# Optimization experiments

Hardware: AMD Instinct MI355X
Metric: run time of the kernel (lower is better)

The kernel has to match this reference:

```python
import jax, jax.numpy as jnp
import numpy as np

N, E, B = 50000, 500000, 2048
IN, ED, H, OUT, P = 64, 16, 64, 64, 1
L, T = 3, 3  # num_layers, num_timesteps
NS = 0.01  # leaky_relu negative slope used throughout AttentiveFP


def _seg_softmax(logits, seg, num):
    # numerically-stable softmax over segments (PyG `softmax`), eps matches PyG
    m = jax.ops.segment_max(logits, seg, num_segments=num)
    e = jnp.exp(logits - m[seg])
    s = jax.ops.segment_sum(e, seg, num_segments=num)
    return e / (s[seg] + 1e-16)


def _gru(xin, h, wx, wh, bx, bh):
    # torch.nn.GRUCell
    gx = xin @ wx.T + bx
    gh = h @ wh.T + bh
    xr, xz, xn = jnp.split(gx, 3, axis=-1)
    hr, hz, hn = jnp.split(gh, 3, axis=-1)
    r = jax.nn.sigmoid(xr + hr)
    z = jax.nn.sigmoid(xz + hz)
    n = jnp.tanh(xn + r * hn)
    return (1.0 - z) * n + z * h


def _forward(x, edge_attr, lin1_w, lin1_b, gate_lin1_w, gate_lin2_w, gate_att_l, gate_att_r, gate_bias,
             gru0_wx, gru0_wh, gru0_bx, gru0_bh,
             atom_lin_w, atom_att_src, atom_att_dst, atom_bias,
             atom_gru_wx, atom_gru_wh, atom_gru_bx, atom_gru_bh,
             mol_lin_w, mol_att_src, mol_att_dst, mol_bias,
             mol_gru_wx, mol_gru_wh, mol_gru_bx, mol_gru_bh,
             lin2_w, lin2_b, ln_g, ln_b, h1_w, h1_b, h2_w, h2_b, h3_w, h3_b,
             edge_index, batch):
    src, dst = edge_index[0], edge_index[1]  # messages flow src -> dst
    x = jax.nn.leaky_relu(x @ lin1_w.T + lin1_b, NS)  # [N, H]
    # --- GATEConv (edge-featured attention) ---
    xj = x[src]  # [E, H]
    e = jax.nn.leaky_relu(jnp.concatenate([xj, edge_attr], axis=-1) @ gate_lin1_w.T, NS)
    alpha = jax.nn.leaky_relu(e @ gate_att_l + x[dst] @ gate_att_r, NS)  # [E]
    alpha = _seg_softmax(alpha, dst, N)
    h = jax.ops.segment_sum((xj @ gate_lin2_w.T) * alpha[:, None], dst, num_segments=N) + gate_bias
    x = jax.nn.relu(_gru(jax.nn.elu(h), x, gru0_wx, gru0_wh, gru0_bx, gru0_bh))
    # --- (num_layers-1) GATConv + GRU layers ---
    for l in range(L - 1):
        xl = x @ atom_lin_w[l].T  # [N, H]
        a = jax.nn.leaky_relu((xl @ atom_att_src[l])[src] + (xl @ atom_att_dst[l])[dst], NS)
        a = _seg_softmax(a, dst, N)
        h = jax.ops.segment_sum(xl[src] * a[:, None], dst, num_segments=N) + atom_bias[l]
        x = jax.nn.relu(_gru(jax.nn.elu(h), x,
                             atom_gru_wx[l], atom_gru_wh[l], atom_gru_bx[l], atom_gru_bh[l]))
    # --- attentive readout over num_timesteps ---
    out = jax.nn.relu(jax.ops.segment_sum(x, batch, num_segments=B))  # [B, H]
    xs = x @ mol_lin_w.T          # bipartite GATConv source transform (fixed)
    a_src = xs @ mol_att_src      # [N]
    for _ in range(T):
        a = jax.nn.leaky_relu(a_src + ((out @ mol_lin_w.T) @ mol_att_dst)[batch], NS)
        a = _seg_softmax(a, batch, B)
        h = jax.nn.elu(jax.ops.segment_sum(xs * a[:, None], batch, num_segments=B) + mol_bias)
        out = jax.nn.relu(_gru(h, out, mol_gru_wx, mol_gru_wh, mol_gru_bx, mol_gru_bh))
    emb = out @ lin2_w.T + lin2_b  # [B, OUT]
    mu = jnp.mean(emb, -1, keepdims=True)
    var = jnp.var(emb, -1, keepdims=True)
    y = (emb - mu) / jnp.sqrt(var + 1e-5) * ln_g + ln_b
    y = jax.nn.relu(y @ h1_w.T + h1_b)
    y = jax.nn.relu(y @ h2_w.T + h2_b)
    return y @ h3_w.T + h3_b  # [B, P]


def setup_inputs() -> dict:
    key = jax.random.key(0)
    ks = iter(jax.random.split(key, 64))
    def w(*s):
        return jax.random.normal(next(ks), s, jnp.float32) * 0.05
    return dict(
        x=jax.random.normal(next(ks), (N, IN), jnp.float32),
        edge_attr=jax.random.normal(next(ks), (E, ED), jnp.float32),
        lin1_w=w(H, IN), lin1_b=w(H),
        gate_lin1_w=w(H, IN + ED), gate_lin2_w=w(H, H),
        gate_att_l=w(H), gate_att_r=w(H), gate_bias=w(H),
        gru0_wx=w(3 * H, H), gru0_wh=w(3 * H, H), gru0_bx=w(3 * H), gru0_bh=w(3 * H),
        atom_lin_w=w(L - 1, H, H), atom_att_src=w(L - 1, H), atom_att_dst=w(L - 1, H), atom_bias=w(L - 1, H),
        atom_gru_wx=w(L - 1, 3 * H, H), atom_gru_wh=w(L - 1, 3 * H, H),
        atom_gru_bx=w(L - 1, 3 * H), atom_gru_bh=w(L - 1, 3 * H),
        mol_lin_w=w(H, H), mol_att_src=w(H), mol_att_dst=w(H), mol_bias=w(H),
        mol_gru_wx=w(3 * H, H), mol_gru_wh=w(3 * H, H), mol_gru_bx=w(3 * H), mol_gru_bh=w(3 * H),
        lin2_w=w(OUT, H), lin2_b=w(OUT),
        ln_g=jnp.ones((OUT,), jnp.float32), ln_b=jnp.zeros((OUT,), jnp.float32),
        h1_w=w(64, OUT), h1_b=w(64), h2_w=w(64, 64), h2_b=w(64), h3_w=w(P, 64), h3_b=w(P),
        edge_index=jax.random.randint(next(ks), (2, E), 0, N, dtype=jnp.int32),
        batch=jnp.sort(jax.random.randint(next(ks), (N,), 0, B, dtype=jnp.int32)),
    )


def reference(x, edge_attr, lin1_w, lin1_b, gate_lin1_w, gate_lin2_w, gate_att_l, gate_att_r, gate_bias, gru0_wx, gru0_wh, gru0_bx, gru0_bh, atom_lin_w, atom_att_src, atom_att_dst, atom_bias, atom_gru_wx, atom_gru_wh, atom_gru_bx, atom_gru_bh, mol_lin_w, mol_att_src, mol_att_dst, mol_bias, mol_gru_wx, mol_gru_wh, mol_gru_bx, mol_gru_bh, lin2_w, lin2_b, ln_g, ln_b, h1_w, h1_b, h2_w, h2_b, h3_w, h3_b, edge_index, batch):
    return _forward(x, edge_attr, lin1_w, lin1_b, gate_lin1_w, gate_lin2_w, gate_att_l, gate_att_r, gate_bias, gru0_wx, gru0_wh, gru0_bx, gru0_bh, atom_lin_w, atom_att_src, atom_att_dst, atom_bias, atom_gru_wx, atom_gru_wh, atom_gru_bx, atom_gru_bh, mol_lin_w, mol_att_src, mol_att_dst, mol_bias, mol_gru_wx, mol_gru_wh, mol_gru_bx, mol_gru_bh, lin2_w, lin2_b, ln_g, ln_b, h1_w, h1_b, h2_w, h2_b, h3_w, h3_b, edge_index, batch)
```

## Files before the change

### kernel.cpp

```cpp
#include <hip/hip_runtime.h>
#include <cfloat>

#define THREADS 256

#define PIN(x) asm volatile("" : "+v"(x))

__device__ __forceinline__ float lrelu01(float v){ return v > 0.f ? v : 0.01f * v; }
__device__ __forceinline__ float reluf(float v){ return v > 0.f ? v : 0.f; }
__device__ __forceinline__ float sigmf(float v){ return 1.f / (1.f + __expf(-v)); }
__device__ __forceinline__ float tanhfast(float v){
    float t = __expf(-2.f * fabsf(v));
    float r = (1.f - t) / (1.f + t);
    return v < 0.f ? -r : r;
}
__device__ __forceinline__ float eluf(float v){ return v > 0.f ? v : __expf(v) - 1.f; }
__device__ __forceinline__ float wmaxf(float v){
    #pragma unroll
    for (int o = 32; o > 0; o >>= 1) v = fmaxf(v, __shfl_xor(v, o, 64));
    return v;
}
__device__ __forceinline__ float wsumf(float v){
    #pragma unroll
    for (int o = 32; o > 0; o >>= 1) v += __shfl_xor(v, o, 64);
    return v;
}

template<int ACT>
__device__ __forceinline__ float actf(float v){
    if (ACT == 1) return lrelu01(v);
    if (ACT == 2) return reluf(v);
    return v;
}

__device__ __forceinline__ void stage_tile(const float* __restrict__ src, float* lds,
                                           int tid, int validf4){
    #pragma unroll
    for (int j = 0; j < 4; ++j){
        int idx = tid + j * 256;
        if (idx < validf4){
            __builtin_amdgcn_global_load_lds(
                (const __attribute__((address_space(1))) void*)(src + (size_t)idx * 4),
                (__attribute__((address_space(3))) void*)(lds + (size_t)idx * 4),
                16, 0, 0);
        }
    }
}

__global__ void k_hist(const int* __restrict__ dst, int* __restrict__ cnt, int E){
    int e = blockIdx.x * blockDim.x + threadIdx.x;
    if (e < E) atomicAdd(&cnt[dst[e]], 1);
}

__global__ void k_scan1(const int* __restrict__ cnt, int* __restrict__ rowptr,
                        int* __restrict__ bsum, int N){
    const int tid = threadIdx.x;
    int i = blockIdx.x * 1024 + tid;
    int v = (i < N) ? cnt[i] : 0;
    int lane = tid & 63, wv = tid >> 6;
    int s = v;
    #pragma unroll
    for (int o = 1; o < 64; o <<= 1){
        int u = __shfl_up(s, o, 64);
        if (lane >= o) s += u;
    }
    __shared__ int wsum[16];
    if (lane == 63) wsum[wv] = s;
    __syncthreads();
    if (wv == 0 && lane < 16){
        int ws = wsum[lane];
        #pragma unroll
        for (int o = 1; o < 16; o <<= 1){
            int u = __shfl_up(ws, o, 64);
            if (lane >= o) ws += u;
        }
        wsum[lane] = ws;
    }
    __syncthreads();
    int woff = wv ? wsum[wv - 1] : 0;
    int incl = s + woff;
    if (i < N) rowptr[i] = incl - v;
    if (tid == 1023) bsum[blockIdx.x] = incl;
}

__global__ void k_scan2(int* __restrict__ bsum, int* __restrict__ rowptr, int NB, int N){
    const int tid = threadIdx.x;
    int v = (tid < NB) ? bsum[tid] : 0;
    int lane = tid & 63, wv = tid >> 6;
    int s = v;
    #pragma unroll
    for (int o = 1; o < 64; o <<= 1){
        int u = __shfl_up(s, o, 64);
        if (lane >= o) s += u;
    }
    __shared__ int wsum[16];
    if (lane == 63) wsum[wv] = s;
    __syncthreads();
    if (wv == 0 && lane < 16){
        int ws = wsum[lane];
        #pragma unroll
        for (int o = 1; o < 16; o <<= 1){
            int u = __shfl_up(ws, o, 64);
            if (lane >= o) ws += u;
        }
        wsum[lane] = ws;
    }
    __syncthreads();
    int woff = wv ? wsum[wv - 1] : 0;
    int incl = s + woff;
    if (tid < NB) bsum[tid] = incl - v;
    if (tid == 1023) rowptr[N] = incl;
}

__global__ void k_scan3(int* __restrict__ rowptr, const int* __restrict__ bsum, int N){
    int i = blockIdx.x * 1024 + threadIdx.x;
    if (i < N) rowptr[i] += bsum[blockIdx.x];
}

__global__ void k_scatter(const int* __restrict__ dst, const int* __restrict__ srcv,
                          const int* __restrict__ rowptr, int* __restrict__ cnt2,
                          int* __restrict__ srcC, int* __restrict__ slot, int E){
    int e = blockIdx.x * blockDim.x + threadIdx.x;
    if (e < E){
        int d = dst[e];
        int p = rowptr[d] + atomicAdd(&cnt2[d], 1);
        srcC[p] = srcv[e];
        slot[e] = p;
    }
}

__global__ void k_browptr(const int* __restrict__ batch, int* __restrict__ rp, int N, int B){
    int n = blockIdx.x * blockDim.x + threadIdx.x;
    if (n >= N) return;
    int b = batch[n];
    int bp = (n == 0) ? -1 : batch[n - 1];
    for (int g = bp + 1; g <= b; ++g) rp[g] = n;
    if (n == N - 1){ for (int g = b + 1; g <= B; ++g) rp[g] = N; }
}

template<int ACT, int NDOT>
__global__ __launch_bounds__(THREADS, 3)
void k_mm64t(const float* __restrict__ in, const float* __restrict__ W, int ldw,
             const float* __restrict__ bias, float* __restrict__ out,
             const float* __restrict__ v0, const float* __restrict__ v1,
             float* __restrict__ o0, float* __restrict__ o1, int rows){
    __shared__ float tile[2][4096];
    const int tid  = threadIdx.x;
    const int lane = tid & 63;
    const int wv   = tid >> 6;
    float w[64];
    #pragma unroll
    for (int k = 0; k < 64; k += 4){
        float4 t4 = *(const float4*)(W + (size_t)lane * ldw + k);
        w[k] = t4.x; w[k+1] = t4.y; w[k+2] = t4.z; w[k+3] = t4.w;
    }
    #pragma unroll
    for (int k = 0; k < 64; ++k) PIN(w[k]);
    const float bb  = bias ? bias[lane] : 0.f;
    const float vl0 = (NDOT > 0) ? v0[lane] : 0.f;
    const float vl1 = (NDOT > 1) ? v1[lane] : 0.f;
    const int ntiles = (rows + 63) >> 6;
    const int totf4  = rows * 16;
    int t = blockIdx.x;
    if (t >= ntiles) return;
    stage_tile(in + (size_t)t * 4096, tile[0], tid, min(1024, totf4 - t * 1024));
    __syncthreads();
    int b = 0;
    while (t < ntiles){
        int tn = t + gridDim.x;
        if (tn < ntiles)
            stage_tile(in + (size_t)tn * 4096, tile[b ^ 1], tid, min(1024, totf4 - tn * 1024));
        #pragma unroll 4
        for (int r = 0; r < 16; ++r){
            int row = wv * 16 + r;
            int g = t * 64 + row;
            const float4* rp = (const float4*)&tile[b][row * 64];
            float a0 = bb, a1 = 0.f, a2 = 0.f, a3 = 0.f;
            #pragma unroll
            for (int kk = 0; kk < 16; ++kk){
                float4 q = rp[kk];
                a0 = fmaf(q.x, w[kk*4],   a0);
                a1 = fmaf(q.y, w[kk*4+1], a1);
                a2 = fmaf(q.z, w[kk*4+2], a2);
                a3 = fmaf(q.w, w[kk*4+3], a3);
            }
            float v = actf<ACT>((a0 + a1) + (a2 + a3));
            if (g < rows){
                out[(size_t)g * 64 + lane] = v;
                if (NDOT > 0){
                    float s0 = wsumf(v * vl0);
                    float s1 = (NDOT > 1) ? wsumf(v * vl1) : 0.f;
                    if (lane == 0){ o0[g] = s0; if (NDOT > 1) o1[g] = s1; }
                }
            }
        }
        __syncthreads();
        b ^= 1; t = tn;
    }
}

__global__ __launch_bounds__(THREADS, 3)
void k_gru_x_t(const float* __restrict__ xin, const float* __restrict__ wx,
               const float* __restrict__ bx,
               float* __restrict__ Rt, float* __restrict__ Zt, float* __restrict__ XN,
               int rows){
    __shared__ float tile[2][4096];
    const int c = blockIdx.y;
    const int tid  = threadIdx.x;
    const int lane = tid & 63;
    const int wv   = tid >> 6;
    float w[64];
    const float* wp = wx + (size_t)(c * 64 + lane) * 64;
    #pragma unroll
    for (int k = 0; k < 64; k += 4){
        float4 t4 = *(const float4*)(wp + k);
        w[k] = t4.x; w[k+1] = t4.y; w[k+2] = t4.z; w[k+3] = t4.w;
    }
    #pragma unroll
    for (int k = 0; k < 64; ++k) PIN(w[k]);
    const float bb = bx[c * 64 + lane];
    float* T = (c == 0) ? Rt : ((c == 1) ? Zt : XN);
    const int ntiles = (rows + 63) >> 6;
    const int totf4  = rows * 16;
    int t = blockIdx.x;
    if (t >= ntiles) return;
    stage_tile(xin + (size_t)t * 4096, tile[0], tid, min(1024, totf4 - t * 1024));
    __syncthreads();
    int b = 0;
    while (t < ntiles){
        int tn = t + gridDim.x;
        if (tn < ntiles)
            stage_tile(xin + (size_t)tn * 4096, tile[b ^ 1], tid, min(1024, totf4 - tn * 1024));
        #pragma unroll 4
        for (int r = 0; r < 16; ++r){
            int row = wv * 16 + r;
            int g = t * 64 + row;
            const float4* rp = (const float4*)&tile[b][row * 64];
            float a0 = bb, a1 = 0.f, a2 = 0.f, a3 = 0.f;
            #pragma unroll
            for (int kk = 0; kk < 16; ++kk){
                float4 q = rp[kk];
                a0 = fmaf(q.x, w[kk*4],   a0);
                a1 = fmaf(q.y, w[kk*4+1], a1);
                a2 = fmaf(q.z, w[kk*4+2], a2);
                a3 = fmaf(q.w, w[kk*4+3], a3);
            }
            if (g < rows) T[(size_t)g * 64 + lane] = (a0 + a1) + (a2 + a3);
        }
        __syncthreads();
        b ^= 1; t = tn;
    }
}

__global__ __launch_bounds__(THREADS, 3)
void k_gru_hsig_t(const float* __restrict__ xp, const float* __restrict__ wh,
                  const float* __restrict__ bh,
                  float* __restrict__ Rt, float* __restrict__ Zt, int rows){
    __shared__ float tile[2][4096];
    const int c = blockIdx.y;
    const int tid  = threadIdx.x;
    const int lane = tid & 63;
    const int wv   = tid >> 6;
    float w[64];
    const float* wp = wh + (size_t)(c * 64 + lane) * 64;
    #pragma unroll
    for (int k = 0; k < 64; k += 4){
        float4 t4 = *(const float4*)(wp + k);
        w[k] = t4.x; w[k+1] = t4.y; w[k+2] = t4.z; w[k+3] = t4.w;
    }
    #pragma unroll
    for (int k = 0; k < 64; ++k) PIN(w[k]);
    const float bb = bh[c * 64 + lane];
    float* T = c ? Zt : Rt;
    const int ntiles = (rows + 63) >> 6;
    const int totf4  = rows * 16;
    int t = blockIdx.x;
    if (t >= ntiles) return;
    stage_tile(xp + (size_t)t * 4096, tile[0], tid, min(1024, totf4 - t * 1024));
    __syncthreads();
    int b = 0;
    while (t < ntiles){
        int tn = t + gridDim.x;
        if (tn < ntiles)
            stage_tile(xp + (size_t)tn * 4096, tile[b ^ 1], tid, min(1024, totf4 - tn * 1024));
        #pragma unroll 4
        for (int r = 0; r < 16; ++r){
            int row = wv * 16 + r;
            int g = t * 64 + row;
            const float4* rp = (const float4*)&tile[b][row * 64];
            float a0 = bb, a1 = 0.f, a2 = 0.f, a3 = 0.f;
            #pragma unroll
            for (int kk = 0; kk < 16; ++kk){
                float4 q = rp[kk];
                a0 = fmaf(q.x, w[kk*4],   a0);
                a1 = fmaf(q.y, w[kk*4+1], a1);
                a2 = fmaf(q.z, w[kk*4+2], a2);
                a3 = fmaf(q.w, w[kk*4+3], a3);
            }
            if (g < rows){
                size_t idx = (size_t)g * 64 + lane;
                T[idx] = sigmf(T[idx] + (a0 + a1) + (a2 + a3));
            }
        }
        __syncthreads();
        b ^= 1; t = tn;
    }
}

__global__ __launch_bounds__(THREADS, 3)
void k_gru_fin3_t(const float* __restrict__ xp, const float* __restrict__ whn,
                  const float* __restrict__ bhn,
                  const float* __restrict__ XN, const float* __restrict__ R,
                  const float* __restrict__ Z, float* __restrict__ out, int rows){
    __shared__ float tile[2][4096];
    const int tid  = threadIdx.x;
    const int lane = tid & 63;
    const int wv   = tid >> 6;
    float w[64];
    #pragma unroll
    for (int k = 0; k < 64; k += 4){
        float4 t4 = *(const float4*)(whn + (size_t)lane * 64 + k);
        w[k] = t4.x; w[k+1] = t4.y; w[k+2] = t4.z; w[k+3] = t4.w;
    }
    #pragma unroll
    for (int k = 0; k < 64; ++k) PIN(w[k]);
    const float bb = bhn[lane];
    const int ntiles = (rows + 63) >> 6;
    const int totf4  = rows * 16;
    int t = blockIdx.x;
    if (t >= ntiles) return;
    stage_tile(xp + (size_t)t * 4096, tile[0], tid, min(1024, totf4 - t * 1024));
    __syncthreads();
    int b = 0;
    while (t < ntiles){
        int tn = t + gridDim.x;
        if (tn < ntiles)
            stage_tile(xp + (size_t)tn * 4096, tile[b ^ 1], tid, min(1024, totf4 - tn * 1024));
        #pragma unroll 4
        for (int r = 0; r < 16; ++r){
            int row = wv * 16 + r;
            int g = t * 64 + row;
            const float4* rp = (const float4*)&tile[b][row * 64];
            float a0 = bb, a1 = 0.f, a2 = 0.f, a3 = 0.f;
            #pragma unroll
            for (int kk = 0; kk < 16; ++kk){
                float4 q = rp[kk];
                a0 = fmaf(q.x, w[kk*4],   a0);
                a1 = fmaf(q.y, w[kk*4+1], a1);
                a2 = fmaf(q.z, w[kk*4+2], a2);
                a3 = fmaf(q.w, w[kk*4+3], a3);
            }
            if (g < rows){
                float hn = (a0 + a1) + (a2 + a3);
                size_t idx = (size_t)g * 64 + lane;
                float rr = R[idx], zz = Z[idx], xn = XN[idx];
                float hp = tile[b][row * 64 + lane];
                float nn = tanhfast(fmaf(rr, hn, xn));
                out[idx] = reluf((1.f - zz) * nn + zz * hp);
            }
        }
        __syncthreads();
        b ^= 1; t = tn;
    }
}

__global__ __launch_bounds__(THREADS, 3)
void k_gate_logit(const float* __restrict__ np1, const float* __restrict__ ea,
                  const float* __restrict__ w1,
                  const float* __restrict__ attl, const float* __restrict__ nat,
                  const int* __restrict__ src, const int* __restrict__ dstv,
                  const int* __restrict__ slot, float* __restrict__ logitC, int E){
    __shared__ float wlds[16 * 64];
    __shared__ float al[64];
    for (int i = threadIdx.x; i < 1024; i += blockDim.x){
        int j = i >> 6, k = i & 63;
        wlds[i] = w1[k * 80 + 64 + j];
    }
    if (threadIdx.x < 64) al[threadIdx.x] = attl[threadIdx.x];
    __syncthreads();
    int e = blockIdx.x * blockDim.x + threadIdx.x;
    if (e >= E) return;
    int s = src[e], d = dstv[e];
    float acc[64];
    const float* nr = np1 + (size_t)s * 64;
    #pragma unroll
    for (int k = 0; k < 64; k += 4){
        float4 t = *(const float4*)(nr + k);
        acc[k] = t.x; acc[k+1] = t.y; acc[k+2] = t.z; acc[k+3] = t.w;
    }
    const float* er = ea + (size_t)e * 16;
    #pragma unroll
    for (int j = 0; j < 16; ++j){
        float v = er[j];
        #pragma unroll
        for (int k = 0; k < 64; k += 4){
            float4 t = *(const float4*)&wlds[j * 64 + k];
            acc[k]   = fmaf(v, t.x, acc[k]);
            acc[k+1] = fmaf(v, t.y, acc[k+1]);
            acc[k+2] = fmaf(v, t.z, acc[k+2]);
            acc[k+3] = fmaf(v, t.w, acc[k+3]);
        }
    }
    float l = 0.f;
    #pragma unroll
    for (int k = 0; k < 64; ++k) l = fmaf(lrelu01(acc[k]), al[k], l);
    logitC[slot[e]] = lrelu01(l + nat[d]);
}

__global__ __launch_bounds__(THREADS, 8)
void k_gate_agg(const float* __restrict__ logitC, const int* __restrict__ srcC,
                const int* __restrict__ rowptr,
// ... 191 lines not shown
    const float* m_gbx   = (const float*)d_in[27];
    const float* m_gbh   = (const float*)d_in[28];
    const float* lin2_w  = (const float*)d_in[29];
    const float* lin2_b  = (const float*)d_in[30];
    const float* ln_g    = (const float*)d_in[31];
    const float* ln_b    = (const float*)d_in[32];
    const float* h1_w    = (const float*)d_in[33];
    const float* h1_b    = (const float*)d_in[34];
    const float* h2_w    = (const float*)d_in[35];
    const float* h2_b    = (const float*)d_in[36];
    const float* h3_w    = (const float*)d_in[37];
    const float* h3_b    = (const float*)d_in[38];
    const int*   ei      = (const int*)d_in[39];
    const int*   batch   = (const int*)d_in[40];
    float* out = (float*)d_out;

    const int N = in_sizes[0] / 64;
    const int E = in_sizes[1] / 16;
    const int P = in_sizes[38];
    const int B = out_size / (P > 0 ? P : 1);
    const int* srcv = ei;
    const int* dstv = ei + E;

    float* Wb = (float*)d_ws;
    size_t nb = (size_t)N * 64;
    size_t bb = (size_t)B * 64;
    float* P0 = Wb;
    float* P1 = P0 + nb;
    float* P2 = P1 + nb;
    float* P3 = P2 + nb;
    float* P4 = P3 + nb;
    float* P5 = P4 + nb;
    float* logitC = P5 + nb;
    float* scal  = logitC + E;
    float* outB0 = scal + 2 * (size_t)N;
    float* outB1 = outB0 + bb;
    float* hB    = outB1 + bb;
    float* RB    = hB + bb;
    float* ZB    = RB + bb;
    float* XNB   = ZB + bb;
    int* srcC   = (int*)(XNB + bb);
    int* slot   = srcC + E;
    int* rowptr = slot + E;
    int* cnt    = rowptr + (N + 1);
    int* cnt2   = cnt + N;
    int* rpB    = cnt2 + N;
    int* bsum   = rpB + (B + 1);
    const int NB = (N + 1023) >> 10;
    size_t need = (size_t)((char*)(bsum + NB) - (char*)d_ws);
    if (need > ws_size) return;
    float* embB = XNB;

    dim3 blk(THREADS);
    int gE    = (E + THREADS - 1) / THREADS;
    int gN4   = (N + 3) / 4;
    int gB4   = (B + 3) / 4;
    int gN256 = (N + THREADS - 1) / THREADS;
    int ntN   = (N + 63) >> 6;
    int ntB   = (B + 63) >> 6;
    int GT_N  = ntN < 768 ? ntN : 768;
    int GT_B  = ntB;

    hipMemsetAsync(cnt, 0, sizeof(int) * 2 * (size_t)N, stream);
    k_hist<<<gE, blk, 0, stream>>>(dstv, cnt, E);
    k_scan1<<<NB, 1024, 0, stream>>>(cnt, rowptr, bsum, N);
    k_scan2<<<1, 1024, 0, stream>>>(bsum, rowptr, NB, N);
    k_scan3<<<NB, 1024, 0, stream>>>(rowptr, bsum, N);
    k_scatter<<<gE, blk, 0, stream>>>(dstv, srcv, rowptr, cnt2, srcC, slot, E);
    k_browptr<<<gN256, blk, 0, stream>>>(batch, rpB, N, B);

    k_mm64t<1,1><<<GT_N, blk, 0, stream>>>(x, lin1_w, 64, lin1_b, P0,
                                           g_attr, nullptr, scal, nullptr, N);

    k_mm64t<0,0><<<GT_N, blk, 0, stream>>>(P0, g_l1w, 80, nullptr, P1,
                                           nullptr, nullptr, nullptr, nullptr, N);
    k_mm64t<0,0><<<GT_N, blk, 0, stream>>>(P0, g_l2w, 64, nullptr, P2,
                                           nullptr, nullptr, nullptr, nullptr, N);
    k_gate_logit<<<gE, blk, 0, stream>>>(P1, eattr, g_l1w, g_attl, scal, srcv, dstv,
                                         slot, logitC, E);
    k_gate_agg<<<gN4, blk, 0, stream>>>(logitC, srcC, rowptr, P2, g_bias, P3, N);
    k_gru_x_t<<<dim3(GT_N, 3), blk, 0, stream>>>(P3, gru0_wx, gru0_bx, P2, P5, P4, N);
    k_gru_hsig_t<<<dim3(GT_N, 2), blk, 0, stream>>>(P0, gru0_wh, gru0_bh, P2, P5, N);
    k_gru_fin3_t<<<GT_N, blk, 0, stream>>>(P0, gru0_wh + 8192, gru0_bh + 128, P4, P2, P5, P1, N);

    k_mm64t<0,2><<<GT_N, blk, 0, stream>>>(P1, a_linw, 64, nullptr, P0,
                                           a_asrc, a_adst, scal, scal + N, N);
    k_atom_agg<<<gN4, blk, 0, stream>>>(scal, scal + N, srcC, rowptr, P0, a_bias, P3, N);
    k_gru_x_t<<<dim3(GT_N, 3), blk, 0, stream>>>(P3, a_gwx, a_gbx, P0, P2, P5, N);
    k_gru_hsig_t<<<dim3(GT_N, 2), blk, 0, stream>>>(P1, a_gwh, a_gbh, P0, P2, N);
    k_gru_fin3_t<<<GT_N, blk, 0, stream>>>(P1, a_gwh + 8192, a_gbh + 128, P5, P0, P2, P4, N);

    k_mm64t<0,2><<<GT_N, blk, 0, stream>>>(P4, a_linw + 4096, 64, nullptr, P0,
                                           a_asrc + 64, a_adst + 64, scal, scal + N, N);
    k_atom_agg<<<gN4, blk, 0, stream>>>(scal, scal + N, srcC, rowptr, P0, a_bias + 64, P3, N);
    k_gru_x_t<<<dim3(GT_N, 3), blk, 0, stream>>>(P3, a_gwx + 12288, a_gbx + 192, P0, P2, P5, N);
    k_gru_hsig_t<<<dim3(GT_N, 2), blk, 0, stream>>>(P4, a_gwh + 12288, a_gbh + 192, P0, P2, N);
    k_gru_fin3_t<<<GT_N, blk, 0, stream>>>(P4, a_gwh + 12288 + 8192, a_gbh + 192 + 128,
                                           P5, P0, P2, P1, N);

    k_mm64t<0,1><<<GT_N, blk, 0, stream>>>(P1, m_linw, 64, nullptr, P0,
                                           m_asrcv, nullptr, scal, nullptr, N);
    k_out0<<<gB4, blk, 0, stream>>>(P1, rpB, outB0, B);
    float* cur = outB0;
    float* nxt = outB1;
    for (int t = 0; t < 3; ++t){
        k_mol_attn<<<gB4, blk, 0, stream>>>(cur, m_linw, m_adstv, scal, P0, rpB, m_bias, hB, B);
        k_gru_x_t<<<dim3(GT_B, 3), blk, 0, stream>>>(hB, m_gwx, m_gbx, RB, ZB, XNB, B);
        k_gru_hsig_t<<<dim3(GT_B, 2), blk, 0, stream>>>(cur, m_gwh, m_gbh, RB, ZB, B);
        k_gru_fin3_t<<<GT_B, blk, 0, stream>>>(cur, m_gwh + 8192, m_gbh + 128, XNB, RB, ZB, nxt, B);
        float* tmp = cur; cur = nxt; nxt = tmp;
    }

    k_mm64t<0,0><<<GT_B, blk, 0, stream>>>(cur, lin2_w, 64, lin2_b, embB,
                                           nullptr, nullptr, nullptr, nullptr, B);
    k_head<<<gB4, blk, 0, stream>>>(embB, ln_g, ln_b, h1_w, h1_b, h2_w, h2_b, h3_w, h3_b, out, B, P);
}
```

Measured before the change: 929.3 us.

## Fuse GRU hidden-gate matmuls and finalize into one kernel; merge dual linear

Replaces the three-kernel GRU pipeline (x-gates, hidden sigmoid gates, n-gate finalize) with two kernels. The first computes all three input-gate projections in one 384-thread block. The second computes all three hidden projections into shared memory and applies the gate math in the same pass, so the R and Z intermediates are no longer written and read back. It also merges the two GATE linear projections over the same input into one kernel and lowers launch_bounds occupancy hints from 3 to 2. The fused kernel uses much more LDS (a 48KB H buffer plus tiles), which may reduce occupancy.

```diff
diff --git a/kernel.cpp b/kernel.cpp
--- a/kernel.cpp
+++ b/kernel.cpp
@@ -38,6 +38,20 @@
     for (int j = 0; j < 4; ++j){
         int idx = tid + j * 256;
         if (idx < validf4){
+            __builtin_amdgcn_global_load_lds(
+                (const __attribute__((address_space(1))) void*)(src + (size_t)idx * 4),
+                (__attribute__((address_space(3))) void*)(lds + (size_t)idx * 4),
+                16, 0, 0);
+        }
+    }
+}
+
+__device__ __forceinline__ void stage_tile384(const float* __restrict__ src, float* lds,
+                                              int tid, int validf4){
+    #pragma unroll
+    for (int j = 0; j < 3; ++j){
+        int idx = tid + j * 384;
+        if (idx < 1024 && idx < validf4){
             __builtin_amdgcn_global_load_lds(
                 (const __attribute__((address_space(1))) void*)(src + (size_t)idx * 4),
                 (__attribute__((address_space(3))) void*)(lds + (size_t)idx * 4),
@@ -138,7 +152,7 @@
 }
 
 template<int ACT, int NDOT>
-__global__ __launch_bounds__(THREADS, 3)
+__global__ __launch_bounds__(THREADS, 2)
 void k_mm64t(const float* __restrict__ in, const float* __restrict__ W, int ldw,
              const float* __restrict__ bias, float* __restrict__ out,
              const float* __restrict__ v0, const float* __restrict__ v1,
@@ -198,41 +212,96 @@
     }
 }
 
-__global__ __launch_bounds__(THREADS, 3)
-void k_gru_x_t(const float* __restrict__ xin, const float* __restrict__ wx,
-               const float* __restrict__ bx,
-               float* __restrict__ Rt, float* __restrict__ Zt, float* __restrict__ XN,
-               int rows){
+__global__ __launch_bounds__(THREADS, 2)
+void k_mm64_x2(const float* __restrict__ in,
+               const float* __restrict__ W0, int ldw0,
+               const float* __restrict__ W1, int ldw1,
+               float* __restrict__ out0, float* __restrict__ out1, int rows){
     __shared__ float tile[2][4096];
-    const int c = blockIdx.y;
     const int tid  = threadIdx.x;
     const int lane = tid & 63;
     const int wv   = tid >> 6;
+    const int osel = wv >> 1;
+    const int rh   = (wv & 1) * 32;
+    const float* W = osel ? W1 : W0;
+    const int ldw  = osel ? ldw1 : ldw0;
+    float* out     = osel ? out1 : out0;
     float w[64];
-    const float* wp = wx + (size_t)(c * 64 + lane) * 64;
     #pragma unroll
     for (int k = 0; k < 64; k += 4){
-        float4 t4 = *(const float4*)(wp + k);
+        float4 t4 = *(const float4*)(W + (size_t)lane * ldw + k);
         w[k] = t4.x; w[k+1] = t4.y; w[k+2] = t4.z; w[k+3] = t4.w;
     }
     #pragma unroll
     for (int k = 0; k < 64; ++k) PIN(w[k]);
-    const float bb = bx[c * 64 + lane];
-    float* T = (c == 0) ? Rt : ((c == 1) ? Zt : XN);
     const int ntiles = (rows + 63) >> 6;
     const int totf4  = rows * 16;
     int t = blockIdx.x;
     if (t >= ntiles) return;
-    stage_tile(xin + (size_t)t * 4096, tile[0], tid, min(1024, totf4 - t * 1024));
+    stage_tile(in + (size_t)t * 4096, tile[0], tid, min(1024, totf4 - t * 1024));
     __syncthreads();
     int b = 0;
     while (t < ntiles){
         int tn = t + gridDim.x;
         if (tn < ntiles)
-            stage_tile(xin + (size_t)tn * 4096, tile[b ^ 1], tid, min(1024, totf4 - tn * 1024));
+            stage_tile(in + (size_t)tn * 4096, tile[b ^ 1], tid, min(1024, totf4 - tn * 1024));
         #pragma unroll 4
-        for (int r = 0; r < 16; ++r){
-            int row = wv * 16 + r;
+        for (int r = 0; r < 32; ++r){
+            int row = rh + r;
+            int g = t * 64 + row;
+            const float4* rp = (const float4*)&tile[b][row * 64];
+            float a0 = 0.f, a1 = 0.f, a2 = 0.f, a3 = 0.f;
+            #pragma unroll
+            for (int kk = 0; kk < 16; ++kk){
+                float4 q = rp[kk];
+                a0 = fmaf(q.x, w[kk*4],   a0);
+                a1 = fmaf(q.y, w[kk*4+1], a1);
+                a2 = fmaf(q.z, w[kk*4+2], a2);
+                a3 = fmaf(q.w, w[kk*4+3], a3);
+            }
+            if (g < rows) out[(size_t)g * 64 + lane] = (a0 + a1) + (a2 + a3);
+        }
+        __syncthreads();
+        b ^= 1; t = tn;
+    }
+}
+
+__global__ __launch_bounds__(384, 2)
+void k_gru_wx(const float* __restrict__ xin, const float* __restrict__ wx,
+              const float* __restrict__ bx,
+              float* __restrict__ Tr, float* __restrict__ Tz, float* __restrict__ Tn,
+              int rows){
+    __shared__ float tile[2][4096];
+    const int tid  = threadIdx.x;
+    const int lane = tid & 63;
+    const int w6   = tid >> 6;
+    const int c    = w6 >> 1;
+    const int rh   = (w6 & 1) * 32;
+    float w[64];
+    const float* wp = wx + (size_t)(c * 64 + lane) * 64;
+    #pragma unroll
+    for (int k = 0; k < 64; k += 4){
+        float4 t4 = *(const float4*)(wp + k);
+        w[k] = t4.x; w[k+1] = t4.y; w[k+2] = t4.z; w[k+3] = t4.w;
+    }
+    #pragma unroll
+    for (int k = 0; k < 64; ++k) PIN(w[k]);
+    const float bb = bx[c * 64 + lane];
+    float* T = (c == 0) ? Tr : ((c == 1) ? Tz : Tn);
+    const int ntiles = (rows + 63) >> 6;
+    const int totf4  = rows * 16;
+    int t = blockIdx.x;
+    if (t >= ntiles) return;
+    stage_tile384(xin + (size_t)t * 4096, tile[0], tid, min(1024, totf4 - t * 1024));
+    __syncthreads();
+    int b = 0;
+    while (t < ntiles){
+        int tn = t + gridDim.x;
+        if (tn < ntiles)
+            stage_tile384(xin + (size_t)tn * 4096, tile[b ^ 1], tid, min(1024, totf4 - tn * 1024));
+        #pragma unroll 4
+        for (int r = 0; r < 32; ++r){
+            int row = rh + r;
             int g = t * 64 + row;
             const float4* rp = (const float4*)&tile[b][row * 64];
             float a0 = bb, a1 = 0.f, a2 = 0.f, a3 = 0.f;
@@ -251,15 +320,18 @@
     }
 }
 
-__global__ __launch_bounds__(THREADS, 3)
-void k_gru_hsig_t(const float* __restrict__ xp, const float* __restrict__ wh,
+__global__ __launch_bounds__(384, 2)
+void k_gru_wh_fin(const float* __restrict__ xp, const float* __restrict__ wh,
                   const float* __restrict__ bh,
-                  float* __restrict__ Rt, float* __restrict__ Zt, int rows){
+                  const float* __restrict__ Tr, const float* __restrict__ Tz,
+                  const float* __restrict__ Tn, float* __restrict__ out, int rows){
     __shared__ float tile[2][4096];
-    const int c = blockIdx.y;
+    __shared__ float H[3][64][64];
     const int tid  = threadIdx.x;
     const int lane = tid & 63;
-    const int wv   = tid >> 6;
+    const int w6   = tid >> 6;
+    const int c    = w6 >> 1;
+    const int rh   = (w6 & 1) * 32;
     float w[64];
     const float* wp = wh + (size_t)(c * 64 + lane) * 64;
     #pragma unroll
@@ -270,22 +342,20 @@
     #pragma unroll
     for (int k = 0; k < 64; ++k) PIN(w[k]);
     const float bb = bh[c * 64 + lane];
-    float* T = c ? Zt : Rt;
     const int ntiles = (rows + 63) >> 6;
     const int totf4  = rows * 16;
     int t = blockIdx.x;
     if (t >= ntiles) return;
-    stage_tile(xp + (size_t)t * 4096, tile[0], tid, min(1024, totf4 - t * 1024));
+    stage_tile384(xp + (size_t)t * 4096, tile[0], tid, min(1024, totf4 - t * 1024));
     __syncthreads();
     int b = 0;
     while (t < ntiles){
         int tn = t + gridDim.x;
         if (tn < ntiles)
-            stage_tile(xp + (size_t)tn * 4096, tile[b ^ 1], tid, min(1024, totf4 - tn * 1024));
+            stage_tile384(xp + (size_t)tn * 4096, tile[b ^ 1], tid, min(1024, totf4 - tn * 1024));
         #pragma unroll 4
-        for (int r = 0; r < 16; ++r){
-            int row = wv * 16 + r;
-            int g = t * 64 + row;
+        for (int r = 0; r < 32; ++r){
+            int row = rh + r;
             const float4* rp = (const float4*)&tile[b][row * 64];
             float a0 = bb, a1 = 0.f, a2 = 0.f, a3 = 0.f;
             #pragma unroll
@@ -296,66 +366,20 @@
                 a2 = fmaf(q.z, w[kk*4+2], a2);
                 a3 = fmaf(q.w, w[kk*4+3], a3);
             }
+            H[c][row][lane] = (a0 + a1) + (a2 + a3);
+        }
+        __syncthreads();
+        int base = t * 64;
+        for (int i = tid; i < 4096; i += 384){
+            int row = i >> 6, col = i & 63;
+            int g = base + row;
             if (g < rows){
-                size_t idx = (size_t)g * 64 + lane;
-                T[idx] = sigmf(T[idx] + (a0 + a1) + (a2 + a3));
-            }
-        }
-        __syncthreads();
-        b ^= 1; t = tn;
-    }
-}
-
-__global__ __launch_bounds__(THREADS, 3)
-void k_gru_fin3_t(const float* __restrict__ xp, const float* __restrict__ whn,
-                  const float* __restrict__ bhn,
-                  const float* __restrict__ XN, const float* __restrict__ R,
-                  const float* __restrict__ Z, float* __restrict__ out, int rows){
-    __shared__ float tile[2][4096];
-    const int tid  = threadIdx.x;
-    const int lane = tid & 63;
-    const int wv   = tid >> 6;
-    float w[64];
-    #pragma unroll
-    for (int k = 0; k < 64; k += 4){
-        float4 t4 = *(const float4*)(whn + (size_t)lane * 64 + k);
-        w[k] = t4.x; w[k+1] = t4.y; w[k+2] = t4.z; w[k+3] = t4.w;
-    }
-    #pragma unroll
-    for (int k = 0; k < 64; ++k) PIN(w[k]);
-    const float bb = bhn[lane];
-    const int ntiles = (rows + 63) >> 6;
-    const int totf4  = rows * 16;
-    int t = blockIdx.x;
-    if (t >= ntiles) return;
-    stage_tile(xp + (size_t)t * 4096, tile[0], tid, min(1024, totf4 - t * 1024));
-    __syncthreads();
-    int b = 0;
-    while (t < ntiles){
-        int tn = t + gridDim.x;
-        if (tn < ntiles)
-            stage_tile(xp + (size_t)tn * 4096, tile[b ^ 1], tid, min(1024, totf4 - tn * 1024));
-        #pragma unroll 4
-        for (int r = 0; r < 16; ++r){
-            int row = wv * 16 + r;
-            int g = t * 64 + row;
-            const float4* rp = (const float4*)&tile[b][row * 64];
-            float a0 = bb, a1 = 0.f, a2 = 0.f, a3 = 0.f;
-            #pragma unroll
-            for (int kk = 0; kk < 16; ++kk){
-                float4 q = rp[kk];
-                a0 = fmaf(q.x, w[kk*4],   a0);
-                a1 = fmaf(q.y, w[kk*4+1], a1);
-                a2 = fmaf(q.z, w[kk*4+2], a2);
-                a3 = fmaf(q.w, w[kk*4+3], a3);
-            }
-            if (g < rows){
-                float hn = (a0 + a1) + (a2 + a3);
-                size_t idx = (size_t)g * 64 + lane;
-                float rr = R[idx], zz = Z[idx], xn = XN[idx];
-                float hp = tile[b][row * 64 + lane];
-                float nn = tanhfast(fmaf(rr, hn, xn));
-                out[idx] = reluf((1.f - zz) * nn + zz * hp);
+                size_t idx = (size_t)g * 64 + col;
+                float r_ = sigmf(Tr[idx] + H[0][row][col]);
+                float z_ = sigmf(Tz[idx] + H[1][row][col]);
+                float nn = tanhfast(fmaf(r_, H[2][row][col], Tn[idx]));
+                float xpv = tile[b][row * 64 + col];
+                out[idx] = reluf((1.f - z_) * nn + z_ * xpv);
             }
         }
         __syncthreads();
@@ -653,6 +677,7 @@
     float* embB = XNB;
 
     dim3 blk(THREADS);
+    dim3 blk384(384);
     int gE    = (E + THREADS - 1) / THREADS;
     int gN4   = (N + 3) / 4;
     int gB4   = (B + 3) / 4;
@@ -660,6 +685,7 @@
     int ntN   = (N + 63) >> 6;
     int ntB   = (B + 63) >> 6;
     int GT_N  = ntN < 768 ? ntN : 768;
+    int GT_N2 = ntN < 512 ? ntN : 512;
     int GT_B  = ntB;
 
     hipMemsetAsync(cnt, 0, sizeof(int) * 2 * (size_t)N, stream);
@@ -673,31 +699,25 @@
     k_mm64t<1,1><<<GT_N, blk, 0, stream>>>(x, lin1_w, 64, lin1_b, P0,
                                            g_attr, nullptr, scal, nullptr, N);
 
-    k_mm64t<0,0><<<GT_N, blk, 0, stream>>>(P0, g_l1w, 80, nullptr, P1,
-                                           nullptr, nullptr, nullptr, nullptr, N);
-    k_mm64t<0,0><<<GT_N, blk, 0, stream>>>(P0, g_l2w, 64, nullptr, P2,
-                                           nullptr, nullptr, nullptr, nullptr, N);
+    k_mm64_x2<<<GT_N, blk, 0, stream>>>(P0, g_l1w, 80, g_l2w, 64, P1, P2, N);
     k_gate_logit<<<gE, blk, 0, stream>>>(P1, eattr, g_l1w, g_attl, scal, srcv, dstv,
                                          slot, logitC, E);
     k_gate_agg<<<gN4, blk, 0, stream>>>(logitC, srcC, rowptr, P2, g_bias, P3, N);
-    k_gru_x_t<<<dim3(GT_N, 3), blk, 0, stream>>>(P3, gru0_wx, gru0_bx, P2, P5, P4, N);
-    k_gru_hsig_t<<<dim3(GT_N, 2), blk, 0, stream>>>(P0, gru0_wh, gru0_bh, P2, P5, N);
-    k_gru_fin3_t<<<GT_N, blk, 0, stream>>>(P0, gru0_wh + 8192, gru0_bh + 128, P4, P2, P5, P1, N);
+    k_gru_wx<<<GT_N, blk384, 0, stream>>>(P3, gru0_wx, gru0_bx, P2, P5, P4, N);
+    k_gru_wh_fin<<<GT_N2, blk384, 0, stream>>>(P0, gru0_wh, gru0_bh, P2, P5, P4, P1, N);
 
     k_mm64t<0,2><<<GT_N, blk, 0, stream>>>(P1, a_linw, 64, nullptr, P0,
                                            a_asrc, a_adst, scal, scal + N, N);
     k_atom_agg<<<gN4, blk, 0, stream>>>(scal, scal + N, srcC, rowptr, P0, a_bias, P3, N);
-    k_gru_x_t<<<dim3(GT_N, 3), blk, 0, stream>>>(P3, a_gwx, a_gbx, P0, P2, P5, N);
-    k_gru_hsig_t<<<dim3(GT_N, 2), blk, 0, stream>>>(P1, a_gwh, a_gbh, P0, P2, N);
-    k_gru_fin3_t<<<GT_N, blk, 0, stream>>>(P1, a_gwh + 8192, a_gbh + 128, P5, P0, P2, P4, N);
+    k_gru_wx<<<GT_N, blk384, 0, stream>>>(P3, a_gwx, a_gbx, P0, P2, P5, N);
+    k_gru_wh_fin<<<GT_N2, blk384, 0, stream>>>(P1, a_gwh, a_gbh, P0, P2, P5, P4, N);
 
     k_mm64t<0,2><<<GT_N, blk, 0, stream>>>(P4, a_linw + 4096, 64, nullptr, P0,
                                            a_asrc + 64, a_adst + 64, scal, scal + N, N);
     k_atom_agg<<<gN4, blk, 0, stream>>>(scal, scal + N, srcC, rowptr, P0, a_bias + 64, P3, N);
-    k_gru_x_t<<<dim3(GT_N, 3), blk, 0, stream>>>(P3, a_gwx + 12288, a_gbx + 192, P0, P2, P5, N);
-    k_gru_hsig_t<<<dim3(GT_N, 2), blk, 0, stream>>>(P4, a_gwh + 12288, a_gbh + 192, P0, P2, N);
-    k_gru_fin3_t<<<GT_N, blk, 0, stream>>>(P4, a_gwh + 12288 + 8192, a_gbh + 192 + 128,
-                                           P5, P0, P2, P1, N);
+    k_gru_wx<<<GT_N, blk384, 0, stream>>>(P3, a_gwx + 12288, a_gbx + 192, P0, P2, P5, N);
+    k_gru_wh_fin<<<GT_N2, blk384, 0, stream>>>(P4, a_gwh + 12288, a_gbh + 192,
+                                               P0, P2, P5, P1, N);
 
     k_mm64t<0,1><<<GT_N, blk, 0, stream>>>(P1, m_linw, 64, nullptr, P0,
                                            m_asrcv, nullptr, scal, nullptr, N);
@@ -706,9 +726,8 @@
     float* nxt = outB1;
     for (int t = 0; t < 3; ++t){
         k_mol_attn<<<gB4, blk, 0, stream>>>(cur, m_linw, m_adstv, scal, P0, rpB, m_bias, hB, B);
-        k_gru_x_t<<<dim3(GT_B, 3), blk, 0, stream>>>(hB, m_gwx, m_gbx, RB, ZB, XNB, B);
-        k_gru_hsig_t<<<dim3(GT_B, 2), blk, 0, stream>>>(cur, m_gwh, m_gbh, RB, ZB, B);
-        k_gru_fin3_t<<<GT_B, blk, 0, stream>>>(cur, m_gwh + 8192, m_gbh + 128, XNB, RB, ZB, nxt, B);
+        k_gru_wx<<<GT_B, blk384, 0, stream>>>(hB, m_gwx, m_gbx, RB, ZB, XNB, B);
+        k_gru_wh_fin<<<GT_B, blk384, 0, stream>>>(cur, m_gwh, m_gbh, RB, ZB, XNB, nxt, B);
         float* tmp = cur; cur = nxt; nxt = tmp;
     }
 
```

After: 995.3 us. 1.07x slower.

## Fuse GRU gate matmuls into two kernels with all gate weights in registers

Applied to the files above, without the earlier changes.

Replaces the three-launch GRU sequence (x-gates, h-sigmoid gates, final n-gate) with two kernels. Each holds all three 64x64 gate weight slices in registers and reads each input tile once instead of once per gate. The final kernel computes r, z and n directly, so the R/Z intermediates are no longer read-modify-written. The two GATE projections sharing P0 are also merged into one kernel. The cost is a much larger per-thread register set (up to 192 weight registers), so launch bounds drop to 2 blocks per CU and grids shrink to 512, which lowers occupancy and risks register spills.

```diff
diff --git a/kernel.cpp b/kernel.cpp
--- a/kernel.cpp
+++ b/kernel.cpp
@@ -138,7 +138,7 @@
 }
 
 template<int ACT, int NDOT>
-__global__ __launch_bounds__(THREADS, 3)
+__global__ __launch_bounds__(THREADS, 2)
 void k_mm64t(const float* __restrict__ in, const float* __restrict__ W, int ldw,
              const float* __restrict__ bias, float* __restrict__ out,
              const float* __restrict__ v0, const float* __restrict__ v1,
@@ -198,27 +198,86 @@
     }
 }
 
-__global__ __launch_bounds__(THREADS, 3)
-void k_gru_x_t(const float* __restrict__ xin, const float* __restrict__ wx,
-               const float* __restrict__ bx,
-               float* __restrict__ Rt, float* __restrict__ Zt, float* __restrict__ XN,
-               int rows){
+__global__ __launch_bounds__(THREADS, 2)
+void k_mm64_x2(const float* __restrict__ in,
+               const float* __restrict__ W0, int ldw0,
+               const float* __restrict__ W1, int ldw1,
+               float* __restrict__ out0, float* __restrict__ out1, int rows){
     __shared__ float tile[2][4096];
-    const int c = blockIdx.y;
     const int tid  = threadIdx.x;
     const int lane = tid & 63;
     const int wv   = tid >> 6;
-    float w[64];
-    const float* wp = wx + (size_t)(c * 64 + lane) * 64;
+    float w0[64], w1[64];
     #pragma unroll
     for (int k = 0; k < 64; k += 4){
-        float4 t4 = *(const float4*)(wp + k);
-        w[k] = t4.x; w[k+1] = t4.y; w[k+2] = t4.z; w[k+3] = t4.w;
-    }
-    #pragma unroll
-    for (int k = 0; k < 64; ++k) PIN(w[k]);
-    const float bb = bx[c * 64 + lane];
-    float* T = (c == 0) ? Rt : ((c == 1) ? Zt : XN);
+        float4 a = *(const float4*)(W0 + (size_t)lane * ldw0 + k);
+        w0[k] = a.x; w0[k+1] = a.y; w0[k+2] = a.z; w0[k+3] = a.w;
+        float4 b4 = *(const float4*)(W1 + (size_t)lane * ldw1 + k);
+        w1[k] = b4.x; w1[k+1] = b4.y; w1[k+2] = b4.z; w1[k+3] = b4.w;
+    }
+    #pragma unroll
+    for (int k = 0; k < 64; ++k){ PIN(w0[k]); PIN(w1[k]); }
+    const int ntiles = (rows + 63) >> 6;
+    const int totf4  = rows * 16;
+    int t = blockIdx.x;
+    if (t >= ntiles) return;
+    stage_tile(in + (size_t)t * 4096, tile[0], tid, min(1024, totf4 - t * 1024));
+    __syncthreads();
+    int b = 0;
+    while (t < ntiles){
+        int tn = t + gridDim.x;
+        if (tn < ntiles)
+            stage_tile(in + (size_t)tn * 4096, tile[b ^ 1], tid, min(1024, totf4 - tn * 1024));
+        #pragma unroll 2
+        for (int r = 0; r < 16; ++r){
+            int row = wv * 16 + r;
+            int g = t * 64 + row;
+            const float4* rp = (const float4*)&tile[b][row * 64];
+            float a0 = 0.f, a1 = 0.f, c0 = 0.f, c1 = 0.f;
+            #pragma unroll
+            for (int kk = 0; kk < 16; ++kk){
+                float4 q = rp[kk];
+                a0 = fmaf(q.x, w0[kk*4],   a0);
+                a1 = fmaf(q.y, w0[kk*4+1], a1);
+                a0 = fmaf(q.z, w0[kk*4+2], a0);
+                a1 = fmaf(q.w, w0[kk*4+3], a1);
+                c0 = fmaf(q.x, w1[kk*4],   c0);
+                c1 = fmaf(q.y, w1[kk*4+1], c1);
+                c0 = fmaf(q.z, w1[kk*4+2], c0);
+                c1 = fmaf(q.w, w1[kk*4+3], c1);
+            }
+            if (g < rows){
+                out0[(size_t)g * 64 + lane] = a0 + a1;
+                out1[(size_t)g * 64 + lane] = c0 + c1;
+            }
+        }
+        __syncthreads();
+        b ^= 1; t = tn;
+    }
+}
+
+__global__ __launch_bounds__(THREADS, 2)
+void k_gru_wx3(const float* __restrict__ xin, const float* __restrict__ wx,
+               const float* __restrict__ bx,
+               float* __restrict__ Tr, float* __restrict__ Tz, float* __restrict__ Tn,
+               int rows){
+    __shared__ float tile[2][4096];
+    const int tid  = threadIdx.x;
+    const int lane = tid & 63;
+    const int wv   = tid >> 6;
+    float wr[64], wz[64], wn[64];
+    #pragma unroll
+    for (int k = 0; k < 64; k += 4){
+        float4 a = *(const float4*)(wx + (size_t)lane * 64 + k);
+        wr[k] = a.x; wr[k+1] = a.y; wr[k+2] = a.z; wr[k+3] = a.w;
+        float4 b4 = *(const float4*)(wx + (size_t)(64 + lane) * 64 + k);
+        wz[k] = b4.x; wz[k+1] = b4.y; wz[k+2] = b4.z; wz[k+3] = b4.w;
+        float4 c4 = *(const float4*)(wx + (size_t)(128 + lane) * 64 + k);
+        wn[k] = c4.x; wn[k+1] = c4.y; wn[k+2] = c4.z; wn[k+3] = c4.w;
+    }
+    #pragma unroll
+    for (int k = 0; k < 64; ++k){ PIN(wr[k]); PIN(wz[k]); PIN(wn[k]); }
+    const float br = bx[lane], bz = bx[64 + lane], bn = bx[128 + lane];
     const int ntiles = (rows + 63) >> 6;
     const int totf4  = rows * 16;
     int t = blockIdx.x;
@@ -230,47 +289,62 @@
         int tn = t + gridDim.x;
         if (tn < ntiles)
             stage_tile(xin + (size_t)tn * 4096, tile[b ^ 1], tid, min(1024, totf4 - tn * 1024));
-        #pragma unroll 4
+        #pragma unroll 2
         for (int r = 0; r < 16; ++r){
             int row = wv * 16 + r;
             int g = t * 64 + row;
             const float4* rp = (const float4*)&tile[b][row * 64];
-            float a0 = bb, a1 = 0.f, a2 = 0.f, a3 = 0.f;
+            float r0 = br, r1 = 0.f, z0 = bz, z1 = 0.f, n0 = bn, n1 = 0.f;
             #pragma unroll
             for (int kk = 0; kk < 16; ++kk){
                 float4 q = rp[kk];
-                a0 = fmaf(q.x, w[kk*4],   a0);
-                a1 = fmaf(q.y, w[kk*4+1], a1);
-                a2 = fmaf(q.z, w[kk*4+2], a2);
-                a3 = fmaf(q.w, w[kk*4+3], a3);
+                r0 = fmaf(q.x, wr[kk*4],   r0);
+                r1 = fmaf(q.y, wr[kk*4+1], r1);
+                r0 = fmaf(q.z, wr[kk*4+2], r0);
+                r1 = fmaf(q.w, wr[kk*4+3], r1);
+                z0 = fmaf(q.x, wz[kk*4],   z0);
+                z1 = fmaf(q.y, wz[kk*4+1], z1);
+                z0 = fmaf(q.z, wz[kk*4+2], z0);
+                z1 = fmaf(q.w, wz[kk*4+3], z1);
+                n0 = fmaf(q.x, wn[kk*4],   n0);
+                n1 = fmaf(q.y, wn[kk*4+1], n1);
+                n0 = fmaf(q.z, wn[kk*4+2], n0);
+                n1 = fmaf(q.w, wn[kk*4+3], n1);
             }
-            if (g < rows) T[(size_t)g * 64 + lane] = (a0 + a1) + (a2 + a3);
+            if (g < rows){
+                size_t idx = (size_t)g * 64 + lane;
+                Tr[idx] = r0 + r1;
+                Tz[idx] = z0 + z1;
+                Tn[idx] = n0 + n1;
+            }
         }
         __syncthreads();
         b ^= 1; t = tn;
     }
 }
 
-__global__ __launch_bounds__(THREADS, 3)
-void k_gru_hsig_t(const float* __restrict__ xp, const float* __restrict__ wh,
-                  const float* __restrict__ bh,
-                  float* __restrict__ Rt, float* __restrict__ Zt, int rows){
+__global__ __launch_bounds__(THREADS, 2)
+void k_gru_whf(const float* __restrict__ xp, const float* __restrict__ wh,
+               const float* __restrict__ bh,
+               const float* __restrict__ Tr, const float* __restrict__ Tz,
+               const float* __restrict__ Tn, float* __restrict__ out, int rows){
     __shared__ float tile[2][4096];
-    const int c = blockIdx.y;
     const int tid  = threadIdx.x;
     const int lane = tid & 63;
     const int wv   = tid >> 6;
-    float w[64];
-    const float* wp = wh + (size_t)(c * 64 + lane) * 64;
+    float wr[64], wz[64], wn[64];
     #pragma unroll
     for (int k = 0; k < 64; k += 4){
-        float4 t4 = *(const float4*)(wp + k);
-        w[k] = t4.x; w[k+1] = t4.y; w[k+2] = t4.z; w[k+3] = t4.w;
-    }
-    #pragma unroll
-    for (int k = 0; k < 64; ++k) PIN(w[k]);
-    const float bb = bh[c * 64 + lane];
-    float* T = c ? Zt : Rt;
+        float4 a = *(const float4*)(wh + (size_t)lane * 64 + k);
+        wr[k] = a.x; wr[k+1] = a.y; wr[k+2] = a.z; wr[k+3] = a.w;
+        float4 b4 = *(const float4*)(wh + (size_t)(64 + lane) * 64 + k);
+        wz[k] = b4.x; wz[k+1] = b4.y; wz[k+2] = b4.z; wz[k+3] = b4.w;
+        float4 c4 = *(const float4*)(wh + (size_t)(128 + lane) * 64 + k);
+        wn[k] = c4.x; wn[k+1] = c4.y; wn[k+2] = c4.z; wn[k+3] = c4.w;
+    }
+    #pragma unroll
+    for (int k = 0; k < 64; ++k){ PIN(wr[k]); PIN(wz[k]); PIN(wn[k]); }
+    const float br = bh[lane], bz = bh[64 + lane], bn = bh[128 + lane];
     const int ntiles = (rows + 63) >> 6;
     const int totf4  = rows * 16;
     int t = blockIdx.x;
@@ -282,80 +356,35 @@
         int tn = t + gridDim.x;
         if (tn < ntiles)
             stage_tile(xp + (size_t)tn * 4096, tile[b ^ 1], tid, min(1024, totf4 - tn * 1024));
-        #pragma unroll 4
+        #pragma unroll 2
         for (int r = 0; r < 16; ++r){
             int row = wv * 16 + r;
             int g = t * 64 + row;
             const float4* rp = (const float4*)&tile[b][row * 64];
-            float a0 = bb, a1 = 0.f, a2 = 0.f, a3 = 0.f;
+            float r0 = br, r1 = 0.f, z0 = bz, z1 = 0.f, n0 = bn, n1 = 0.f;
             #pragma unroll
             for (int kk = 0; kk < 16; ++kk){
                 float4 q = rp[kk];
-                a0 = fmaf(q.x, w[kk*4],   a0);
-                a1 = fmaf(q.y, w[kk*4+1], a1);
-                a2 = fmaf(q.z, w[kk*4+2], a2);
-                a3 = fmaf(q.w, w[kk*4+3], a3);
+                r0 = fmaf(q.x, wr[kk*4],   r0);
+                r1 = fmaf(q.y, wr[kk*4+1], r1);
+                r0 = fmaf(q.z, wr[kk*4+2], r0);
+                r1 = fmaf(q.w, wr[kk*4+3], r1);
+                z0 = fmaf(q.x, wz[kk*4],   z0);
+                z1 = fmaf(q.y, wz[kk*4+1], z1);
+                z0 = fmaf(q.z, wz[kk*4+2], z0);
+                z1 = fmaf(q.w, wz[kk*4+3], z1);
+                n0 = fmaf(q.x, wn[kk*4],   n0);
+                n1 = fmaf(q.y, wn[kk*4+1], n1);
+                n0 = fmaf(q.z, wn[kk*4+2], n0);
+                n1 = fmaf(q.w, wn[kk*4+3], n1);
             }
             if (g < rows){
                 size_t idx = (size_t)g * 64 + lane;
-                T[idx] = sigmf(T[idx] + (a0 + a1) + (a2 + a3));
-            }
-        }
-        __syncthreads();
-        b ^= 1; t = tn;
-    }
-}
-
-__global__ __launch_bounds__(THREADS, 3)
-void k_gru_fin3_t(const float* __restrict__ xp, const float* __restrict__ whn,
-                  const float* __restrict__ bhn,
-                  const float* __restrict__ XN, const float* __restrict__ R,
-                  const float* __restrict__ Z, float* __restrict__ out, int rows){
-    __shared__ float tile[2][4096];
-    const int tid  = threadIdx.x;
-    const int lane = tid & 63;
-    const int wv   = tid >> 6;
-    float w[64];
-    #pragma unroll
-    for (int k = 0; k < 64; k += 4){
-        float4 t4 = *(const float4*)(whn + (size_t)lane * 64 + k);
-        w[k] = t4.x; w[k+1] = t4.y; w[k+2] = t4.z; w[k+3] = t4.w;
-    }
-    #pragma unroll
-    for (int k = 0; k < 64; ++k) PIN(w[k]);
-    const float bb = bhn[lane];
-    const int ntiles = (rows + 63) >> 6;
-    const int totf4  = rows * 16;
-    int t = blockIdx.x;
-    if (t >= ntiles) return;
-    stage_tile(xp + (size_t)t * 4096, tile[0], tid, min(1024, totf4 - t * 1024));
-    __syncthreads();
-    int b = 0;
-    while (t < ntiles){
-        int tn = t + gridDim.x;
-        if (tn < ntiles)
-            stage_tile(xp + (size_t)tn * 4096, tile[b ^ 1], tid, min(1024, totf4 - tn * 1024));
-        #pragma unroll 4
-        for (int r = 0; r < 16; ++r){
-            int row = wv * 16 + r;
-            int g = t * 64 + row;
-            const float4* rp = (const float4*)&tile[b][row * 64];
-            float a0 = bb, a1 = 0.f, a2 = 0.f, a3 = 0.f;
-            #pragma unroll
-            for (int kk = 0; kk < 16; ++kk){
-                float4 q = rp[kk];
-                a0 = fmaf(q.x, w[kk*4],   a0);
-                a1 = fmaf(q.y, w[kk*4+1], a1);
-                a2 = fmaf(q.z, w[kk*4+2], a2);
-                a3 = fmaf(q.w, w[kk*4+3], a3);
-            }
-            if (g < rows){
-                float hn = (a0 + a1) + (a2 + a3);
-                size_t idx = (size_t)g * 64 + lane;
-                float rr = R[idx], zz = Z[idx], xn = XN[idx];
-                float hp = tile[b][row * 64 + lane];
-                float nn = tanhfast(fmaf(rr, hn, xn));
-                out[idx] = reluf((1.f - zz) * nn + zz * hp);
+                float r_ = sigmf(Tr[idx] + (r0 + r1));
+                float z_ = sigmf(Tz[idx] + (z0 + z1));
+                float nn = tanhfast(fmaf(r_, n0 + n1, Tn[idx]));
+                float xpv = tile[b][row * 64 + lane];
+                out[idx] = reluf((1.f - z_) * nn + z_ * xpv);
             }
         }
         __syncthreads();
@@ -660,6 +689,7 @@
     int ntN   = (N + 63) >> 6;
     int ntB   = (B + 63) >> 6;
     int GT_N  = ntN < 768 ? ntN : 768;
+    int GT_N2 = ntN < 512 ? ntN : 512;
     int GT_B  = ntB;
 
     hipMemsetAsync(cnt, 0, sizeof(int) * 2 * (size_t)N, stream);
@@ -673,31 +703,24 @@
     k_mm64t<1,1><<<GT_N, blk, 0, stream>>>(x, lin1_w, 64, lin1_b, P0,
                                            g_attr, nullptr, scal, nullptr, N);
 
-    k_mm64t<0,0><<<GT_N, blk, 0, stream>>>(P0, g_l1w, 80, nullptr, P1,
-                                           nullptr, nullptr, nullptr, nullptr, N);
-    k_mm64t<0,0><<<GT_N, blk, 0, stream>>>(P0, g_l2w, 64, nullptr, P2,
-                                           nullptr, nullptr, nullptr, nullptr, N);
+    k_mm64_x2<<<GT_N2, blk, 0, stream>>>(P0, g_l1w, 80, g_l2w, 64, P1, P2, N);
     k_gate_logit<<<gE, blk, 0, stream>>>(P1, eattr, g_l1w, g_attl, scal, srcv, dstv,
                                          slot, logitC, E);
     k_gate_agg<<<gN4, blk, 0, stream>>>(logitC, srcC, rowptr, P2, g_bias, P3, N);
-    k_gru_x_t<<<dim3(GT_N, 3), blk, 0, stream>>>(P3, gru0_wx, gru0_bx, P2, P5, P4, N);
-    k_gru_hsig_t<<<dim3(GT_N, 2), blk, 0, stream>>>(P0, gru0_wh, gru0_bh, P2, P5, N);
-    k_gru_fin3_t<<<GT_N, blk, 0, stream>>>(P0, gru0_wh + 8192, gru0_bh + 128, P4, P2, P5, P1, N);
+    k_gru_wx3<<<GT_N2, blk, 0, stream>>>(P3, gru0_wx, gru0_bx, P2, P5, P4, N);
+    k_gru_whf<<<GT_N2, blk, 0, stream>>>(P0, gru0_wh, gru0_bh, P2, P5, P4, P1, N);
 
     k_mm64t<0,2><<<GT_N, blk, 0, stream>>>(P1, a_linw, 64, nullptr, P0,
                                            a_asrc, a_adst, scal, scal + N, N);
     k_atom_agg<<<gN4, blk, 0, stream>>>(scal, scal + N, srcC, rowptr, P0, a_bias, P3, N);
-    k_gru_x_t<<<dim3(GT_N, 3), blk, 0, stream>>>(P3, a_gwx, a_gbx, P0, P2, P5, N);
-    k_gru_hsig_t<<<dim3(GT_N, 2), blk, 0, stream>>>(P1, a_gwh, a_gbh, P0, P2, N);
-    k_gru_fin3_t<<<GT_N, blk, 0, stream>>>(P1, a_gwh + 8192, a_gbh + 128, P5, P0, P2, P4, N);
+    k_gru_wx3<<<GT_N2, blk, 0, stream>>>(P3, a_gwx, a_gbx, P0, P2, P5, N);
+    k_gru_whf<<<GT_N2, blk, 0, stream>>>(P1, a_gwh, a_gbh, P0, P2, P5, P4, N);
 
     k_mm64t<0,2><<<GT_N, blk, 0, stream>>>(P4, a_linw + 4096, 64, nullptr, P0,
                                            a_asrc + 64, a_adst + 64, scal, scal + N, N);
     k_atom_agg<<<gN4, blk, 0, stream>>>(scal, scal + N, srcC, rowptr, P0, a_bias + 64, P3, N);
-    k_gru_x_t<<<dim3(GT_N, 3), blk, 0, stream>>>(P3, a_gwx + 12288, a_gbx + 192, P0, P2, P5, N);
-    k_gru_hsig_t<<<dim3(GT_N, 2), blk, 0, stream>>>(P4, a_gwh + 12288, a_gbh + 192, P0, P2, N);
-    k_gru_fin3_t<<<GT_N, blk, 0, stream>>>(P4, a_gwh + 12288 + 8192, a_gbh + 192 + 128,
-                                           P5, P0, P2, P1, N);
+    k_gru_wx3<<<GT_N2, blk, 0, stream>>>(P3, a_gwx + 12288, a_gbx + 192, P0, P2, P5, N);
+    k_gru_whf<<<GT_N2, blk, 0, stream>>>(P4, a_gwh + 12288, a_gbh + 192, P0, P2, P5, P1, N);
 
     k_mm64t<0,1><<<GT_N, blk, 0, stream>>>(P1, m_linw, 64, nullptr, P0,
                                            m_asrcv, nullptr, scal, nullptr, N);
@@ -706,9 +729,8 @@
     float* nxt = outB1;
     for (int t = 0; t < 3; ++t){
         k_mol_attn<<<gB4, blk, 0, stream>>>(cur, m_linw, m_adstv, scal, P0, rpB, m_bias, hB, B);
-        k_gru_x_t<<<dim3(GT_B, 3), blk, 0, stream>>>(hB, m_gwx, m_gbx, RB, ZB, XNB, B);
-        k_gru_hsig_t<<<dim3(GT_B, 2), blk, 0, stream>>>(cur, m_gwh, m_gbh, RB, ZB, B);
-        k_gru_fin3_t<<<GT_B, blk, 0, stream>>>(cur, m_gwh + 8192, m_gbh + 128, XNB, RB, ZB, nxt, B);
+        k_gru_wx3<<<GT_B, blk, 0, stream>>>(hB, m_gwx, m_gbx, RB, ZB, XNB, B);
+        k_gru_whf<<<GT_B, blk, 0, stream>>>(cur, m_gwh, m_gbh, RB, ZB, XNB, nxt, B);
         float* tmp = cur; cur = nxt; nxt = tmp;
     }
 
```

Result: faster. 781.9 us (-15.9%).
